# Kernel optimization log

Measured on AMD Instinct MI355X. Metric: run time of the kernel, lower is better.

Reference implementation:

```python
import math
import jax, jax.numpy as jnp
import numpy as np

H = 2048      # hidden_size
NH = 16       # num_attention_heads
QL = 1536     # q_lora_rank
KVL = 512     # kv_lora_rank
NOPE = 128    # qk_nope_head_dim
ROPE = 64     # qk_rope_head_dim
VD = 128      # v_head_dim
QKH = NOPE + ROPE
B, S = 2, 2048
EPS = 1e-6
MIN_VAL = -1e15


def _rms_norm(x, w, eps=EPS):
    var = jnp.mean(x * x, axis=-1, keepdims=True)
    return w * (x * jax.lax.rsqrt(var + eps))


def _rotate_half(x):
    x1, x2 = jnp.split(x, 2, axis=-1)
    return jnp.concatenate((-x2, x1), axis=-1)


def _rope_tables(seq_len, dim):
    inv_freq = 1.0 / (10000.0 ** (np.arange(0, dim, 2, dtype=np.float32) / dim))
    t = np.arange(seq_len, dtype=np.float32)[:, None]
    freqs = t @ inv_freq[None, :]
    freqs = np.concatenate((freqs, freqs), axis=-1)  # [S, dim]
    return jnp.asarray(np.cos(freqs)), jnp.asarray(np.sin(freqs))


def setup_inputs() -> dict:
    key = jax.random.key(0)
    ks = jax.random.split(key, 16)
    s = 0.02
    inp = {
        "x": jax.random.normal(ks[0], (B, S, H), dtype=jnp.float32),
        "mask": jnp.ones((B, S), dtype=jnp.int32),
        "wq_a_w": jax.random.normal(ks[1], (QL, H), dtype=jnp.float32) * s,
        "wq_a_b": jnp.zeros((QL,), dtype=jnp.float32),
        "q_norm_w": jnp.ones((QL,), dtype=jnp.float32),
        "wq_b_w": jax.random.normal(ks[2], (NH * QKH, QL), dtype=jnp.float32) * s,
        "wq_b_b": jnp.zeros((NH * QKH,), dtype=jnp.float32),
        "wkv_a_w": jax.random.normal(ks[3], (KVL + ROPE, H), dtype=jnp.float32) * s,
        "wkv_a_b": jnp.zeros((KVL + ROPE,), dtype=jnp.float32),
        "kv_norm_w": jnp.ones((KVL,), dtype=jnp.float32),
        "wkv_b_w": jax.random.normal(ks[4], (NH * (NOPE + VD), KVL), dtype=jnp.float32) * s,
        "wo_w": jax.random.normal(ks[5], (H, NH * VD), dtype=jnp.float32) * s,
        "wo_b": jnp.zeros((H,), dtype=jnp.float32),
    }
    return inp


def reference(x, mask, wq_a_w, wq_a_b, q_norm_w, wq_b_w, wq_b_b,
              wkv_a_w, wkv_a_b, kv_norm_w, wkv_b_w, wo_w, wo_b):
    bs, seq, _ = x.shape
    # ---- low-rank Q path ----
    q = x @ wq_a_w.T + wq_a_b                 # [b,s,QL]
    q = _rms_norm(q, q_norm_w)
    q = q @ wq_b_w.T + wq_b_b                 # [b,s,NH*QKH]
    q = q.reshape(bs, seq, NH, QKH)
    q_nope, q_pe = q[..., :NOPE], q[..., NOPE:]
    # ---- low-rank KV path ----
    kv_full = x @ wkv_a_w.T + wkv_a_b          # [b,s,KVL+ROPE]
    kv, k_pe = kv_full[..., :KVL], kv_full[..., KVL:]
    kv = _rms_norm(kv, kv_norm_w)              # latent kv cache [b,s,KVL]
    # ---- RoPE on the small rope slice only ----
    cos, sin = _rope_tables(seq, ROPE)         # [s,ROPE]
    cos_q, sin_q = cos[None, :, None, :], sin[None, :, None, :]
    q_pe = q_pe * cos_q + _rotate_half(q_pe) * sin_q            # [b,s,NH,ROPE]
    k_pe = k_pe * cos[None, :, :] + _rotate_half(k_pe) * sin[None, :, :]  # [b,s,ROPE]
    # ---- weight absorption ----
    wkv_b = wkv_b_w.reshape(NH, NOPE + VD, KVL)
    q_lat = jnp.einsum('bshd,hdc->bshc', q_nope, wkv_b[:, :NOPE])  # absorb W_UK
    scores = (jnp.einsum('bshc,btc->bsht', q_lat, kv)
              + jnp.einsum('bshr,btr->bsht', q_pe, k_pe)) / math.sqrt(QKH)
    # ---- causal + padding mask ----
    causal = jnp.triu(jnp.full((seq, seq), MIN_VAL, dtype=scores.dtype), k=1)
    m = jnp.where(mask[:, None, :] == 0, MIN_VAL, causal[None])    # [b,s,t]
    scores = scores + m[:, :, None, :]
    attn = jax.nn.softmax(scores, axis=-1)                         # [b,s,h,t]
    out = jnp.einsum('bsht,btc->bshc', attn, kv)                   # latent values
    out = jnp.einsum('bshc,hdc->bshd', out, wkv_b[:, NOPE:])       # absorb W_UV
    out = out.reshape(bs, seq, NH * VD) @ wo_w.T + wo_b
    return out
```

## Files before the change

kernel.cpp:

```cpp
#include <hip/hip_runtime.h>
#include <hip/hip_bf16.h>

#define BB   2
#define SS   2048
#define HH   2048
#define NHH  16
#define QLL  1536
#define KVLL 512
#define NOPE_D 128
#define ROPE_D 64
#define QKH_D  192
#define VD_D   128
#define MROWS  (BB*SS)

typedef __attribute__((ext_vector_type(8))) short bf16x8;
typedef __attribute__((ext_vector_type(4))) float f32x4;

__device__ inline float bf2f(unsigned short u) {
    union { float f; unsigned int i; } v; v.i = ((unsigned int)u) << 16; return v.f;
}
__device__ inline unsigned short f2bf(float f) {
    union { float f; unsigned int u; } v; v.f = f;
    unsigned int r = v.u + 0x7fffu + ((v.u >> 16) & 1u);
    return (unsigned short)(r >> 16);
}

__device__ __forceinline__ void gload_lds16(const ushort* g, ushort* l)
{
    __builtin_amdgcn_global_load_lds(
        (const __attribute__((address_space(1))) void*)(g),
        (__attribute__((address_space(3))) void*)(l), 16, 0, 0);
}

__global__ void conv6(const float* s0, ushort* d0, int n0,
                      const float* s1, ushort* d1, int n1,
                      const float* s2, ushort* d2, int n2,
                      const float* s3, ushort* d3, int n3,
                      const float* s4, ushort* d4, int n4,
                      const float* s5, ushort* d5, int n5)
{
    const int st = gridDim.x * 256;
    const int t0 = blockIdx.x * 256 + threadIdx.x;
    for (int i = t0; i < n0; i += st) { float4 v = ((const float4*)s0)[i]; ushort4 u; u.x=f2bf(v.x);u.y=f2bf(v.y);u.z=f2bf(v.z);u.w=f2bf(v.w); ((ushort4*)d0)[i]=u; }
    for (int i = t0; i < n1; i += st) { float4 v = ((const float4*)s1)[i]; ushort4 u; u.x=f2bf(v.x);u.y=f2bf(v.y);u.z=f2bf(v.z);u.w=f2bf(v.w); ((ushort4*)d1)[i]=u; }
    for (int i = t0; i < n2; i += st) { float4 v = ((const float4*)s2)[i]; ushort4 u; u.x=f2bf(v.x);u.y=f2bf(v.y);u.z=f2bf(v.z);u.w=f2bf(v.w); ((ushort4*)d2)[i]=u; }
    for (int i = t0; i < n3; i += st) { float4 v = ((const float4*)s3)[i]; ushort4 u; u.x=f2bf(v.x);u.y=f2bf(v.y);u.z=f2bf(v.z);u.w=f2bf(v.w); ((ushort4*)d3)[i]=u; }
    for (int i = t0; i < n4; i += st) { float4 v = ((const float4*)s4)[i]; ushort4 u; u.x=f2bf(v.x);u.y=f2bf(v.y);u.z=f2bf(v.z);u.w=f2bf(v.w); ((ushort4*)d4)[i]=u; }
    for (int i = t0; i < n5; i += st) { float4 v = ((const float4*)s5)[i]; ushort4 u; u.x=f2bf(v.x);u.y=f2bf(v.y);u.z=f2bf(v.z);u.w=f2bf(v.w); ((ushort4*)d5)[i]=u; }
}

template<typename TC>
__launch_bounds__(256, 3)
__global__ void gemm_bf(const ushort* __restrict__ A, int lda, size_t Ab, size_t Ah,
                        const ushort* __restrict__ B, int ldb, size_t Bb, size_t Bh,
                        const float* __restrict__ bias,
                        TC* __restrict__ C, int ldc, size_t Cb, size_t Ch,
                        int M, int N, int K)
{
    __shared__ ushort As[128 * 64];
    __shared__ ushort Bs[128 * 64];
    const int z = blockIdx.z, bz = z >> 4, hz = z & 15;
    A += (size_t)bz * Ab + (size_t)hz * Ah;
    B += (size_t)bz * Bb + (size_t)hz * Bh;
    C += (size_t)bz * Cb + (size_t)hz * Ch;
    int bx = blockIdx.x, by = blockIdx.y;
    if (gridDim.z == 1) {
        const int gx = gridDim.x, nwg = gx * gridDim.y;
        if ((nwg & 7) == 0) {
            int lin = by * gx + bx;
            int swz = (lin & 7) * (nwg >> 3) + (lin >> 3);
            bx = swz % gx; by = swz / gx;
        }
    }
    const int m0 = by * 128, n0 = bx * 128;
    const int tid = threadIdx.x, w = tid >> 6, lane = tid & 63;
    const int l15 = lane & 15, q = lane >> 4;
    const int r7 = lane >> 3, c7 = lane & 7;
    const int xork = l15 & 7;

    f32x4 acc[4][4];
#pragma unroll
    for (int i = 0; i < 4; i++)
#pragma unroll
        for (int j = 0; j < 4; j++) acc[i][j] = (f32x4){0.f, 0.f, 0.f, 0.f};

    const int mrow = 64 * (w & 1) + l15;
    const int nrow = 64 * (w >> 1) + l15;

    for (int k0 = 0; k0 < K; k0 += 64) {
#pragma unroll
        for (int i = 0; i < 4; i++) {
            int g = 4 * w + i;
            int row = g * 8 + r7;
            int ch = c7 ^ r7;
            gload_lds16(A + (size_t)(m0 + row) * lda + k0 + ch * 8,
                        As + g * 512 + lane * 8);
            int rb = n0 + row; if (rb > N - 1) rb = N - 1;
            gload_lds16(B + (size_t)rb * ldb + k0 + ch * 8,
                        Bs + g * 512 + lane * 8);
        }
        __syncthreads();
#pragma unroll
        for (int ks = 0; ks < 2; ks++) {
            bf16x8 af[4], bf[4];
            const int chx = (ks * 4 + q) ^ xork;
#pragma unroll
            for (int mt = 0; mt < 4; mt++)
                af[mt] = *(const bf16x8*)(As + (mrow + 16 * mt) * 64 + chx * 8);
#pragma unroll
            for (int nt = 0; nt < 4; nt++)
                bf[nt] = *(const bf16x8*)(Bs + (nrow + 16 * nt) * 64 + chx * 8);
#pragma unroll
            for (int mt = 0; mt < 4; mt++)
#pragma unroll
                for (int nt = 0; nt < 4; nt++)
                    acc[mt][nt] = __builtin_amdgcn_mfma_f32_16x16x32_bf16(af[mt], bf[nt], acc[mt][nt], 0, 0, 0);
        }
        __syncthreads();
    }

#pragma unroll
    for (int nt = 0; nt < 4; nt++) {
        int n = n0 + nrow + 16 * nt;
        if (n >= N) continue;
        float bv = bias ? bias[n] : 0.f;
#pragma unroll
        for (int mt = 0; mt < 4; mt++) {
#pragma unroll
            for (int r = 0; r < 4; r++) {
                int m = m0 + 64 * (w & 1) + 16 * mt + 4 * q + r;
                float v = acc[mt][nt][r] + bv;
                if constexpr (sizeof(TC) == 2) C[(size_t)m * ldc + n] = f2bf(v);
                else                           C[(size_t)m * ldc + n] = v;
            }
        }
    }
}

__launch_bounds__(256)
__global__ void rmsnorm_bf16(ushort* __restrict__ x, const float* __restrict__ w, int width)
{
    ushort* xr = x + (size_t)blockIdx.x * width;
    float ss = 0.f;
    for (int i = threadIdx.x; i < width; i += 256) { float v = bf2f(xr[i]); ss += v * v; }
    __shared__ float red[256];
    red[threadIdx.x] = ss; __syncthreads();
    for (int off = 128; off > 0; off >>= 1) {
        if (threadIdx.x < off) red[threadIdx.x] += red[threadIdx.x + off];
        __syncthreads();
    }
    float r = rsqrtf(red[0] / (float)width + 1e-6f);
    for (int i = threadIdx.x; i < width; i += 256)
        xr[i] = f2bf(w[i] * bf2f(xr[i]) * r);
}

__device__ inline float rope_val(float xj, float xo, int j, int s)
{
    int i = j & 31;
    float freq = powf(10000.f, -(float)i / 32.f);
    float a = (float)s * freq;
    float sn, cs; sincosf(a, &sn, &cs);
    float other = (j < 32) ? -xo : xo;
    return xj * cs + other * sn;
}

__launch_bounds__(256)
__global__ void finalize_kv(const ushort* __restrict__ kvf, const float* __restrict__ w,
                            ushort* __restrict__ kvbf)
{
    int m = blockIdx.x, s = m & (SS - 1);
    const ushort* xr = kvf + (size_t)m * 576;
    float ss = 0.f;
    for (int i = threadIdx.x; i < 512; i += 256) { float v = bf2f(xr[i]); ss += v * v; }
    __shared__ float red[256];
    red[threadIdx.x] = ss; __syncthreads();
    for (int off = 128; off > 0; off >>= 1) {
        if (threadIdx.x < off) red[threadIdx.x] += red[threadIdx.x + off];
        __syncthreads();
    }
    float r = rsqrtf(red[0] / 512.f + 1e-6f);
    for (int i = threadIdx.x; i < 512; i += 256)
        kvbf[(size_t)m * 576 + i] = f2bf(w[i] * bf2f(xr[i]) * r);
    if (threadIdx.x < 64) {
        int j = threadIdx.x;
        float xj = bf2f(xr[512 + j]), xo = bf2f(xr[512 + (j ^ 32)]);
        kvbf[(size_t)m * 576 + 512 + j] = f2bf(rope_val(xj, xo, j, s));
    }
}

__global__ void rope_q_kernel(ushort* __restrict__ qbuf)
{
    int m = blockIdx.x, s = m & (SS - 1);
    int w = threadIdx.x >> 6, j = threadIdx.x & 63;
    int h = blockIdx.y * 4 + w;
    ushort* p = qbuf + (size_t)m * 3072 + h * QKH_D + NOPE_D;
    float xj = bf2f(p[j]);
    float xo = bf2f(p[j ^ 32]);
    p[j] = f2bf(rope_val(xj, xo, j, s));
}

#define SCL  0.10411760f
#define PTL  72
#define NJOB 45

__constant__ unsigned char JQT[NJOB] = {18,17,16,19,20,21,22,23,24,25,26,27,28,29,30,31,15,31,14,30,13,29,12,28,11,27,10,26,9,25,8,24,7,23,6,22,5,21,4,20,3,19,2,1,0};
__constant__ unsigned char JT0[NJOB] = { 0, 0, 0, 0, 0, 0, 0, 0, 0, 0, 0, 0, 0, 0, 0, 0, 0,16, 0,16, 0,16, 0,16, 0,16, 0,16, 0,16, 0,16, 0,16, 0,16, 0,16, 0,16, 0,16, 0, 0, 0};
__constant__ unsigned char JT1[NJOB] = {19,18,17,16,16,16,16,16,16,16,16,16,16,16,16,16,16,32,15,31,14,30,13,29,12,28,11,27,10,26, 9,25, 8,24, 7,23, 6,22, 5,21, 4,20, 3, 2, 1};

__device__ __forceinline__ int ktidx(int row, int ch) {
    return (((ch >> 3) << 3) + (row >> 3)) * 512 + (row & 7) * 64 + (((ch & 7) ^ (row & 7)) << 3);
}
__device__ __forceinline__ int vtidx(int d, int ch) {
    return (d >> 3) * 512 + (d & 7) * 64 + ((ch ^ (d & 7)) << 3);
}

__launch_bounds__(256, 3)
__global__ void attn_mfma(const ushort* __restrict__ qbuf, const ushort* __restrict__ Kf,
                          const ushort* __restrict__ kvbf, const ushort* __restrict__ VT,
                          const int* __restrict__ mask, ushort* __restrict__ o_heads,
                          ushort* __restrict__ Opart, float2* __restrict__ mlbuf)
{
    __shared__ ushort Kt[24 * 512];
    __shared__ ushort Vt[16 * 512];
    __shared__ ushort Pt[4 * 16 * PTL];

    const int tid = threadIdx.x, w = tid >> 6, lane = tid & 63;
    const int l15 = lane & 15, q = lane >> 4;
    const int r7 = lane >> 3, c7 = lane & 7;

    const int job = blockIdx.x >> 5, bh = blockIdx.x & 31;
    const int b = bh >> 4, h = bh & 15;
    const int qt = JQT[job], t0s = JT0[job], t1s = JT1[job];
    const int s0 = qt * 64;
    const bool partial = (t0s != 0) | (t1s != qt + 1);

    const ushort* Kf_bh = Kf + (size_t)bh * SS * NOPE_D;
    const ushort* VT_bh = VT + (size_t)bh * VD_D * SS;
    const ushort* kpe_b = kvbf + (size_t)b * SS * 576 + 512;
    const int* mrow = mask + b * SS;
    ushort* Ptw = Pt + w * 16 * PTL;

    bf16x8 qf[6];
    {
        const ushort* qbase = qbuf + ((size_t)(b * SS) + s0 + 16 * w + l15) * 3072 + h * QKH_D + q * 8;
#pragma unroll
        for (int k = 0; k < 6; k++) qf[k] = *(const bf16x8*)(qbase + k * 32);
    }

    f32x4 Oacc[8];
#pragma unroll
    for (int nt = 0; nt < 8; nt++) Oacc[nt] = (f32x4){0.f, 0.f, 0.f, 0.f};
    float m_i = -3e38f, l_i = 0.f;
    const int my_s = s0 + 16 * w + l15;

    for (int st = t0s; st < t1s; st++) {
        const int t0 = st * 64;
#pragma unroll
        for (int i = 0; i < 6; i++) {
            int g = 6 * w + i;
            int rg = g & 7, cg = g >> 3;
            int row = rg * 8 + r7;
            int chl = c7 ^ r7;
            const ushort* src = (cg < 2)
                ? Kf_bh + (size_t)(t0 + row) * NOPE_D + (cg * 8 + chl) * 8
                : kpe_b + (size_t)(t0 + row) * 576 + chl * 8;
            gload_lds16(src, Kt + g * 512 + lane * 8);
        }
#pragma unroll
        for (int i = 0; i < 4; i++) {
            int g = 4 * w + i;
            int d = g * 8 + r7;
            gload_lds16(VT_bh + (size_t)d * SS + t0 + ((c7 ^ r7) << 3),
                        Vt + g * 512 + lane * 8);
        }
        __syncthreads();
        f32x4 sa[4];
#pragma unroll
        for (int c = 0; c < 4; c++) sa[c] = (f32x4){0.f, 0.f, 0.f, 0.f};
        __builtin_amdgcn_s_setprio(1);
#pragma unroll
        for (int k = 0; k < 6; k++) {
#pragma unroll
            for (int c = 0; c < 4; c++) {
                bf16x8 kb = *(const bf16x8*)(Kt + ktidx(16 * c + l15, 4 * k + q));
                sa[c] = __builtin_amdgcn_mfma_f32_16x16x32_bf16(kb, qf[k], sa[c], 0, 0, 0);
            }
        }
        __builtin_amdgcn_s_setprio(0);
        float sc[4][4];
#pragma unroll
        for (int c = 0; c < 4; c++) {
            int4 mv4 = *(const int4*)&mrow[t0 + 16 * c + 4 * q];
#pragma unroll
            for (int r = 0; r < 4; r++) {
                int t = t0 + 16 * c + 4 * q + r;
                float v = sa[c][r] * SCL;
                int mvr = (&mv4.x)[r];
                if (t > my_s || mvr == 0) v = -1e30f;
                sc[c][r] = v;
            }
        }
        float mx = fmaxf(
            fmaxf(fmaxf(fmaxf(sc[0][0], sc[0][1]), fmaxf(sc[0][2], sc[0][3])),
                  fmaxf(fmaxf(sc[1][0], sc[1][1]), fmaxf(sc[1][2], sc[1][3]))),
            fmaxf(fmaxf(fmaxf(sc[2][0], sc[2][1]), fmaxf(sc[2][2], sc[2][3])),
                  fmaxf(fmaxf(sc[3][0], sc[3][1]), fmaxf(sc[3][2], sc[3][3]))));
        mx = fmaxf(mx, __shfl_xor(mx, 16));
        mx = fmaxf(mx, __shfl_xor(mx, 32));
        float mn = fmaxf(m_i, mx);
        if (!__all(mx <= m_i)) {
            float alpha = exp2f(m_i - mn);
            l_i *= alpha;
#pragma unroll
            for (int nt = 0; nt < 8; nt++) {
                Oacc[nt][0] *= alpha; Oacc[nt][1] *= alpha;
                Oacc[nt][2] *= alpha; Oacc[nt][3] *= alpha;
            }
        }
        m_i = mn;
        float ps = 0.f;
#pragma unroll
        for (int c = 0; c < 4; c++) {
            ushort4 pk;
#pragma unroll
            for (int r = 0; r < 4; r++) {
                float p = exp2f(sc[c][r] - mn);
                ps += p;
                (&pk.x)[r] = f2bf(p);
            }
            *(ushort4*)(Ptw + l15 * PTL + 16 * c + 4 * q) = pk;
        }
        ps += __shfl_xor(ps, 16);
        ps += __shfl_xor(ps, 32);
        l_i += ps;
        bf16x8 pb[2];
#pragma unroll
        for (int kt = 0; kt < 2; kt++)
            pb[kt] = *(const bf16x8*)(Ptw + l15 * PTL + kt * 32 + q * 8);
        __builtin_amdgcn_s_setprio(1);
#pragma unroll
        for (int nt = 0; nt < 8; nt++) {
#pragma unroll
            for (int kt = 0; kt < 2; kt++) {
                bf16x8 vf = *(const bf16x8*)(Vt + vtidx(16 * nt + l15, kt * 4 + q));
                Oacc[nt] = __builtin_amdgcn_mfma_f32_16x16x32_bf16(vf, pb[kt], Oacc[nt], 0, 0, 0);
            }
        }
        __builtin_amdgcn_s_setprio(0);
        __syncthreads();
    }

    float lv = (l_i > 0.f) ? 1.f / l_i : 0.f;

    if (!partial) {
        ushort* orow = o_heads + (size_t)(b * SS + my_s) * 2048 + h * VD_D;
#pragma unroll
        for (int nt = 0; nt < 8; nt++) {
            ushort4 pk;
            pk.x = f2bf(Oacc[nt][0] * lv); pk.y = f2bf(Oacc[nt][1] * lv);
            pk.z = f2bf(Oacc[nt][2] * lv); pk.w = f2bf(Oacc[nt][3] * lv);
            *(ushort4*)(orow + 16 * nt + 4 * q) = pk;
        }
    } else {
        const int sp = (t0s != 0);
        const int p = bh * 26 + (qt - 19) * 2 + sp;
        const int rl = 16 * w + l15;
        ushort* prow = Opart + ((size_t)p * 64 + rl) * 128;
#pragma unroll
        for (int nt = 0; nt < 8; nt++) {
            ushort4 pk;
            pk.x = f2bf(Oacc[nt][0] * lv); pk.y = f2bf(Oacc[nt][1] * lv);
            pk.z = f2bf(Oacc[nt][2] * lv); pk.w = f2bf(Oacc[nt][3] * lv);
            *(ushort4*)(prow + 16 * nt + 4 * q) = pk;
        }
        if (lane < 16)
            mlbuf[p * 64 + rl] = make_float2(m_i, l_i);
    }
}

__launch_bounds__(256)
__global__ void attn_merge(const ushort* __restrict__ Opart, const float2* __restrict__ mlbuf,
                           ushort* __restrict__ o_heads)
{
    int bh = blockIdx.x & 31, qi = blockIdx.x >> 5;
    int b = bh >> 4, h = bh & 15;
    int qt = 19 + qi;
    int t = threadIdx.x;
    int row = t >> 2, dbase = (t & 3) * 32;
    int p0 = bh * 26 + qi * 2, p1 = p0 + 1;
    float2 ml0 = mlbuf[p0 * 64 + row], ml1 = mlbuf[p1 * 64 + row];
    float M = fmaxf(ml0.x, ml1.x);
    float w0 = (ml0.y > 0.f) ? exp2f(ml0.x - M) * ml0.y : 0.f;
    float w1 = (ml1.y > 0.f) ? exp2f(ml1.x - M) * ml1.y : 0.f;
    float den = w0 + w1;
    float inv = (den > 0.f) ? 1.f / den : 0.f;
    w0 *= inv; w1 *= inv;
    int s = qt * 64 + row;
    const ushort* O0 = Opart + ((size_t)p0 * 64 + row) * 128 + dbase;
    const ushort* O1 = Opart + ((size_t)p1 * 64 + row) * 128 + dbase;
    ushort* dst = o_heads + (size_t)(b * SS + s) * 2048 + h * VD_D + dbase;
#pragma unroll
    for (int c = 0; c < 32; c += 8) {
        bf16x8 a = *(const bf16x8*)(O0 + c);
        bf16x8 bb = *(const bf16x8*)(O1 + c);
        bf16x8 o;
#pragma unroll
        for (int j = 0; j < 8; j++)
            o[j] = (short)f2bf(w0 * bf2f((unsigned short)a[j]) + w1 * bf2f((unsigned short)bb[j]));
        *(bf16x8*)(dst + c) = o;
    }
}

extern "C" void kernel_launch(void* const* d_in, const int* in_sizes, int n_in,
                              void* d_out, int out_size, void* d_ws, size_t ws_size,
                              hipStream_t stream)
{
    const float* x        = (const float*)d_in[0];
    const int*   mask     = (const int*)d_in[1];
    const float* wq_a_w   = (const float*)d_in[2];
    const float* wq_a_b   = (const float*)d_in[3];
    const float* q_norm_w = (const float*)d_in[4];
    const float* wq_b_w   = (const float*)d_in[5];
    const float* wq_b_b   = (const float*)d_in[6];
    const float* wkv_a_w  = (const float*)d_in[7];
    const float* wkv_a_b  = (const float*)d_in[8];
    const float* kv_norm_w= (const float*)d_in[9];
    const float* wkv_b_w  = (const float*)d_in[10];
    const float* wo_w     = (const float*)d_in[11];
    const float* wo_b     = (const float*)d_in[12];
    float* out = (float*)d_out;

    char* W = (char*)d_ws;
    ushort* wo_bf    = (ushort*)(W + 0);
    ushort* qbuf     = (ushort*)(W + 8388608);
    ushort* wq_b_bf  = (ushort*)(W + 33554432);
    ushort* Kf       = (ushort*)(W + 33554432);
    ushort* wq_a_bf  = (ushort*)(W + 42991616);
    ushort* kvfull_bf= (ushort*)(W + 42991616);
    ushort* x_bf     = (ushort*)(W + 50331648);
    ushort* VT       = (ushort*)(W + 50331648);
    ushort* q_a_bf   = (ushort*)(W + 67108864);
    ushort* o_heads  = (ushort*)(W + 67108864);
    ushort* wkv_a_bf = (ushort*)(W + 79691776);
    ushort* wkv_b_bf = (ushort*)(W + 83886080);
    ushort* Opart    = (ushort*)(W + 83886080);
    float2* mlbuf    = (float2*)(W + 97517568);
    ushort* kvbf     = (ushort*)(W + 97943552);

    conv6<<<4096, 256, 0, stream>>>(
        x, x_bf, MROWS * HH / 4,
        wq_a_w, wq_a_bf, QLL * HH / 4,
        wq_b_w, wq_b_bf, 3072 * QLL / 4,
        wkv_a_w, wkv_a_bf, 576 * HH / 4,
        wkv_b_w, wkv_b_bf, NHH * 256 * 512 / 4,
        wo_w, wo_bf, HH * 2048 / 4);

    gemm_bf<ushort><<<dim3(QLL/128, MROWS/128, 1), 256, 0, stream>>>(
        x_bf, HH, 0, 0, wq_a_bf, HH, 0, 0, wq_a_b, q_a_bf, QLL, 0, 0, MROWS, QLL, HH);
    rmsnorm_bf16<<<MROWS, 256, 0, stream>>>(q_a_bf, q_norm_w, QLL);
    gemm_bf<ushort><<<dim3(3072/128, MROWS/128, 1), 256, 0, stream>>>(
        q_a_bf, QLL, 0, 0, wq_b_bf, QLL, 0, 0, wq_b_b, qbuf, 3072, 0, 0, MROWS, 3072, QLL);
    gemm_bf<ushort><<<dim3(5, MROWS/128, 1), 256, 0, stream>>>(
        x_bf, HH, 0, 0, wkv_a_bf, HH, 0, 0, wkv_a_b, kvfull_bf, 576, 0, 0, MROWS, 576, HH);
    finalize_kv<<<MROWS, 256, 0, stream>>>(kvfull_bf, kv_norm_w, kvbf);
    rope_q_kernel<<<dim3(MROWS, 4), 256, 0, stream>>>(qbuf);
    gemm_bf<ushort><<<dim3(1, SS/128, 32), 256, 0, stream>>>(
        kvbf, 576, (size_t)SS * 576, 0,
        wkv_b_bf, 512, 0, (size_t)256 * 512,
        nullptr, Kf, NOPE_D, (size_t)NHH * SS * NOPE_D, (size_t)SS * NOPE_D,
        SS, NOPE_D, 512);
    gemm_bf<ushort><<<dim3(SS/128, 1, 32), 256, 0, stream>>>(
        wkv_b_bf + (size_t)128 * 512, 512, 0, (size_t)256 * 512,
        kvbf, 576, (size_t)SS * 576, 0,
        nullptr, VT, SS, (size_t)NHH * VD_D * SS, (size_t)VD_D * SS,
        VD_D, SS, 512);
    attn_mfma<<<NJOB * 32, 256, 0, stream>>>(qbuf, Kf, kvbf, VT, mask, o_heads, Opart, mlbuf);
    attn_merge<<<13 * 32, 256, 0, stream>>>(Opart, mlbuf, o_heads);
    gemm_bf<float><<<dim3(HH/128, MROWS/128, 1), 256, 0, stream>>>(
        o_heads, NHH * VD_D, 0, 0, wo_bf, NHH * VD_D, 0, 0, wo_b, out, HH, 0, 0,
        MROWS, HH, NHH * VD_D);
}
```

Baseline: 479.1 us.

## Vectorize norms, skip causal check off-diagonal, use packed bf16 convert, drop GEMM swizzle

```diff
diff --git a/kernel.cpp b/kernel.cpp
--- a/kernel.cpp
+++ b/kernel.cpp
@@ -24,6 +24,11 @@
     unsigned int r = v.u + 0x7fffu + ((v.u >> 16) & 1u);
     return (unsigned short)(r >> 16);
 }
+__device__ __forceinline__ unsigned int cvtpk(float lo, float hi) {
+    unsigned int r;
+    asm("v_cvt_pk_bf16_f32 %0, %1, %2" : "=v"(r) : "v"(lo), "v"(hi));
+    return r;
+}
 
 __device__ __forceinline__ void gload_lds16(const ushort* g, ushort* l)
 {
@@ -63,16 +68,7 @@
     A += (size_t)bz * Ab + (size_t)hz * Ah;
     B += (size_t)bz * Bb + (size_t)hz * Bh;
     C += (size_t)bz * Cb + (size_t)hz * Ch;
-    int bx = blockIdx.x, by = blockIdx.y;
-    if (gridDim.z == 1) {
-        const int gx = gridDim.x, nwg = gx * gridDim.y;
-        if ((nwg & 7) == 0) {
-            int lin = by * gx + bx;
-            int swz = (lin & 7) * (nwg >> 3) + (lin >> 3);
-            bx = swz % gx; by = swz / gx;
-        }
-    }
-    const int m0 = by * 128, n0 = bx * 128;
+    const int m0 = blockIdx.y * 128, n0 = blockIdx.x * 128;
     const int tid = threadIdx.x, w = tid >> 6, lane = tid & 63;
     const int l15 = lane & 15, q = lane >> 4;
     const int r7 = lane >> 3, c7 = lane & 7;
@@ -141,8 +137,13 @@
 __global__ void rmsnorm_bf16(ushort* __restrict__ x, const float* __restrict__ w, int width)
 {
     ushort* xr = x + (size_t)blockIdx.x * width;
+    const int w4 = width >> 2;
     float ss = 0.f;
-    for (int i = threadIdx.x; i < width; i += 256) { float v = bf2f(xr[i]); ss += v * v; }
+    for (int i = threadIdx.x; i < w4; i += 256) {
+        ushort4 v = ((const ushort4*)xr)[i];
+        float a = bf2f(v.x), b = bf2f(v.y), c = bf2f(v.z), d = bf2f(v.w);
+        ss += (a * a + b * b) + (c * c + d * d);
+    }
     __shared__ float red[256];
     red[threadIdx.x] = ss; __syncthreads();
     for (int off = 128; off > 0; off >>= 1) {
@@ -150,8 +151,16 @@
         __syncthreads();
     }
     float r = rsqrtf(red[0] / (float)width + 1e-6f);
-    for (int i = threadIdx.x; i < width; i += 256)
-        xr[i] = f2bf(w[i] * bf2f(xr[i]) * r);
+    for (int i = threadIdx.x; i < w4; i += 256) {
+        ushort4 v = ((const ushort4*)xr)[i];
+        float4 wv = ((const float4*)w)[i];
+        ushort4 o;
+        o.x = f2bf(wv.x * bf2f(v.x) * r);
+        o.y = f2bf(wv.y * bf2f(v.y) * r);
+        o.z = f2bf(wv.z * bf2f(v.z) * r);
+        o.w = f2bf(wv.w * bf2f(v.w) * r);
+        ((ushort4*)xr)[i] = o;
+    }
 }
 
 __device__ inline float rope_val(float xj, float xo, int j, int s)
@@ -171,7 +180,11 @@
     int m = blockIdx.x, s = m & (SS - 1);
     const ushort* xr = kvf + (size_t)m * 576;
     float ss = 0.f;
-    for (int i = threadIdx.x; i < 512; i += 256) { float v = bf2f(xr[i]); ss += v * v; }
+    for (int i = threadIdx.x; i < 128; i += 256) {
+        ushort4 v = ((const ushort4*)xr)[i];
+        float a = bf2f(v.x), b = bf2f(v.y), c = bf2f(v.z), d = bf2f(v.w);
+        ss += (a * a + b * b) + (c * c + d * d);
+    }
     __shared__ float red[256];
     red[threadIdx.x] = ss; __syncthreads();
     for (int off = 128; off > 0; off >>= 1) {
@@ -179,12 +192,21 @@
         __syncthreads();
     }
     float r = rsqrtf(red[0] / 512.f + 1e-6f);
-    for (int i = threadIdx.x; i < 512; i += 256)
-        kvbf[(size_t)m * 576 + i] = f2bf(w[i] * bf2f(xr[i]) * r);
+    ushort* dr = kvbf + (size_t)m * 576;
+    for (int i = threadIdx.x; i < 128; i += 256) {
+        ushort4 v = ((const ushort4*)xr)[i];
+        float4 wv = ((const float4*)w)[i];
+        ushort4 o;
+        o.x = f2bf(wv.x * bf2f(v.x) * r);
+        o.y = f2bf(wv.y * bf2f(v.y) * r);
+        o.z = f2bf(wv.z * bf2f(v.z) * r);
+        o.w = f2bf(wv.w * bf2f(v.w) * r);
+        ((ushort4*)dr)[i] = o;
+    }
     if (threadIdx.x < 64) {
         int j = threadIdx.x;
         float xj = bf2f(xr[512 + j]), xo = bf2f(xr[512 + (j ^ 32)]);
-        kvbf[(size_t)m * 576 + 512 + j] = f2bf(rope_val(xj, xo, j, s));
+        dr[512 + j] = f2bf(rope_val(xj, xo, j, s));
     }
 }
 
@@ -288,16 +310,28 @@
         }
         __builtin_amdgcn_s_setprio(0);
         float sc[4][4];
-#pragma unroll
-        for (int c = 0; c < 4; c++) {
-            int4 mv4 = *(const int4*)&mrow[t0 + 16 * c + 4 * q];
-#pragma unroll
-            for (int r = 0; r < 4; r++) {
-                int t = t0 + 16 * c + 4 * q + r;
-                float v = sa[c][r] * SCL;
-                int mvr = (&mv4.x)[r];
-                if (t > my_s || mvr == 0) v = -1e30f;
-                sc[c][r] = v;
+        if (st == qt) {
+#pragma unroll
+            for (int c = 0; c < 4; c++) {
+                int4 mv4 = *(const int4*)&mrow[t0 + 16 * c + 4 * q];
+#pragma unroll
+                for (int r = 0; r < 4; r++) {
+                    int t = t0 + 16 * c + 4 * q + r;
+                    float v = sa[c][r] * SCL;
+                    if (t > my_s || (&mv4.x)[r] == 0) v = -1e30f;
+                    sc[c][r] = v;
+                }
+            }
+        } else {
+#pragma unroll
+            for (int c = 0; c < 4; c++) {
+                int4 mv4 = *(const int4*)&mrow[t0 + 16 * c + 4 * q];
+#pragma unroll
+                for (int r = 0; r < 4; r++) {
+                    float v = sa[c][r] * SCL;
+                    if ((&mv4.x)[r] == 0) v = -1e30f;
+                    sc[c][r] = v;
+                }
             }
         }
         float mx = fmaxf(
@@ -321,14 +355,15 @@
         float ps = 0.f;
 #pragma unroll
         for (int c = 0; c < 4; c++) {
-            ushort4 pk;
-#pragma unroll
-            for (int r = 0; r < 4; r++) {
-                float p = exp2f(sc[c][r] - mn);
-                ps += p;
-                (&pk.x)[r] = f2bf(p);
-            }
-            *(ushort4*)(Ptw + l15 * PTL + 16 * c + 4 * q) = pk;
+            float p0 = exp2f(sc[c][0] - mn);
+            float p1 = exp2f(sc[c][1] - mn);
+            float p2 = exp2f(sc[c][2] - mn);
+            float p3 = exp2f(sc[c][3] - mn);
+            ps += (p0 + p1) + (p2 + p3);
+            uint2 pk2;
+            pk2.x = cvtpk(p0, p1);
+            pk2.y = cvtpk(p2, p3);
+            *(uint2*)(Ptw + l15 * PTL + 16 * c + 4 * q) = pk2;
         }
         ps += __shfl_xor(ps, 16);
         ps += __shfl_xor(ps, 32);
```

Measured after the change: 478.0 us. No clear change (-0.2%).
